# Performance work log

Measured on AMD Instinct MI355X. Metric: run time of the kernel, lower is better.

Reference implementation:

```python
import jax, jax.numpy as jnp
import numpy as np

# dims: T tokens, E experts, D model dim, F ffn dim, C per-expert capacity, K top-k routing
T, E, D, F, C, K = 4096, 8, 1024, 4096, 1536, 2


def setup_inputs() -> dict:
    key = jax.random.key(0)
    k_x, k_lg, k_w1, k_w2 = jax.random.split(key, 4)
    x = jax.random.normal(k_x, (T, D), jnp.float32)
    # external router: top-K of logits per token, softmax weights over kept logits
    logits = jax.random.normal(k_lg, (T, E), jnp.float32)
    topv, topi = jax.lax.top_k(logits, K)                      # (T,K)
    rows = jnp.arange(T)[:, None]
    route_mask = jnp.zeros((T, E), bool).at[rows, topi].set(True)
    route_weight = jnp.zeros((T, E), jnp.float32).at[rows, topi].set(
        jax.nn.softmax(topv, axis=-1))
    # stacked homogeneous expert MLP params (E leading axis, as in _stack_group)
    W1 = jax.random.normal(k_w1, (E, D, F), jnp.float32) / np.sqrt(D)
    b1 = jnp.zeros((E, F), jnp.float32)
    W2 = jax.random.normal(k_w2, (E, F, D), jnp.float32) / np.sqrt(F)
    b2 = jnp.zeros((E, D), jnp.float32)
    return dict(x=x, route_mask=route_mask, route_weight=route_weight,
                W1=W1, b1=b1, W2=W2, b2=b2)


def reference(x, route_mask, route_weight, W1, b1, W2, b2):
    """MoE with per-expert capacity: top-C tokens per expert by route weight,
    gather -> vmapped expert MLP -> weighted scatter-combine.
    Math identical to the one-hot slot einsums ('ect,t...->ec...' dispatch and
    'ecf,ect,te->tf' combine) of the original, expressed as gather/scatter.
    """
    Tn, En = route_mask.shape
    w_te = jnp.where(route_mask, route_weight, 0.0)            # (T,E)
    # per-expert scores; unrouted tokens get -inf so they can never be selected
    w_et = jnp.where(route_mask.T, w_te.T, -jnp.inf)           # (E,T)
    vals, idx = jax.lax.top_k(w_et, C)                         # (E,C) token ids per slot
    valid = jnp.isfinite(vals)                                  # slot actually filled
    # dispatch: gather token features into (E,C,D); empty slots are zero rows
    xe = x[idx] * valid[..., None]
    # grouped expert MLP (vmap over E via batched einsum)
    h = jax.nn.relu(jnp.einsum('ecd,edf->ecf', xe, W1) + b1[:, None, :])
    out = jnp.einsum('ecf,efd->ecd', h, W2) + b2[:, None, :]    # (E,C,D)
    # combine: y[t] = sum over slots assigned to t of w_te[t,e] * out[e,c]
    gain = jnp.where(valid, jnp.take_along_axis(w_te.T, idx, axis=1), 0.0)  # (E,C)
    y = jnp.zeros((Tn, out.shape[-1]), out.dtype)
    y = y.at[idx.reshape(-1)].add((out * gain[..., None]).reshape(-1, out.shape[-1]))
    return y
```

## Files before the change

kernel.cpp:

```cpp
#include <hip/hip_runtime.h>
#include <hip/hip_bf16.h>
#include <stdint.h>

#define T_TOK 4096
#define NE    8
#define DM    1024
#define FF    4096
#define CAP   1536

typedef __attribute__((ext_vector_type(8))) __bf16 bf16x8;
typedef __attribute__((ext_vector_type(4))) float  f32x4;

__device__ __forceinline__ void gload_lds16(const void* gptr, void* lptr) {
  __builtin_amdgcn_global_load_lds(
      (__attribute__((address_space(1))) void*)(uintptr_t)gptr,
      (__attribute__((address_space(3))) void*)(uintptr_t)lptr,
      16, 0, 0);
}


__global__ void conv_x_kernel(const float4* __restrict__ src, ushort4* __restrict__ dst, int n4) {
  int i = blockIdx.x * blockDim.x + threadIdx.x;
  if (i >= n4) return;
  float4 v = src[i];
  ushort4 o;
  o.x = __builtin_bit_cast(unsigned short, __float2bfloat16(v.x));
  o.y = __builtin_bit_cast(unsigned short, __float2bfloat16(v.y));
  o.z = __builtin_bit_cast(unsigned short, __float2bfloat16(v.z));
  o.w = __builtin_bit_cast(unsigned short, __float2bfloat16(v.w));
  dst[i] = o;
}

__global__ __launch_bounds__(256)
void tconv_kernel(const float* __restrict__ src, __hip_bfloat16* __restrict__ dst,
                  int R, int C) {
  __shared__ float tile[64][65];
  const int b  = blockIdx.z;
  const int r0 = blockIdx.y * 64;
  const int c0 = blockIdx.x * 64;
  const float* s = src + (size_t)b * R * C;
  __hip_bfloat16* d = dst + (size_t)b * R * C;
  const int tid = threadIdx.x;
  const int tx = tid & 63, ty = tid >> 6;
#pragma unroll
  for (int rr = ty; rr < 64; rr += 4)
    tile[rr][tx] = s[(size_t)(r0 + rr) * C + c0 + tx];
  __syncthreads();
  const int lg = tid & 15;
  const int cg = tid >> 4;
#pragma unroll
  for (int w = 0; w < 4; ++w) {
    const int cc = w * 16 + cg;
    const int r4 = lg * 4;
    ushort4 o;
    o.x = __builtin_bit_cast(unsigned short, __float2bfloat16(tile[r4 + 0][cc]));
    o.y = __builtin_bit_cast(unsigned short, __float2bfloat16(tile[r4 + 1][cc]));
    o.z = __builtin_bit_cast(unsigned short, __float2bfloat16(tile[r4 + 2][cc]));
    o.w = __builtin_bit_cast(unsigned short, __float2bfloat16(tile[r4 + 3][cc]));
    *(ushort4*)&d[(size_t)(c0 + cc) * R + r0 + r4] = o;
  }
}

__global__ void router_kernel(const float* __restrict__ rw, int* __restrict__ counts,
                              int* __restrict__ tok_ids, float* __restrict__ gains) {
  int t = blockIdx.x * blockDim.x + threadIdx.x;
  if (t >= T_TOK) return;
#pragma unroll
  for (int e = 0; e < NE; ++e) {
    float w = rw[t * NE + e];
    if (w > 0.f) {
      int pos = atomicAdd(&counts[e], 1);
      if (pos < CAP) {
        tok_ids[e * CAP + pos] = t;
        gains[e * CAP + pos]   = w;
      }
    }
  }
}

__global__ void pad_kernel(const int* __restrict__ counts, int* __restrict__ tok_ids,
                           float* __restrict__ gains) {
  int i = blockIdx.x * blockDim.x + threadIdx.x;
  if (i >= NE * CAP) return;
  int e = i / CAP, pos = i % CAP;
  int ne = min(counts[e], CAP);
  if (pos >= ne) { tok_ids[i] = 0; gains[i] = 0.f; }
}


template <int PASS>
__global__ __launch_bounds__(256, 3)
void moe_gemm(const __hip_bfloat16* __restrict__ Asrc,
              const __hip_bfloat16* __restrict__ Bsrc,
              const float* __restrict__ bias,
              const int* __restrict__ counts,
              const int* __restrict__ tok_ids,
              const float* __restrict__ gains,
              __hip_bfloat16* __restrict__ Hout,
              float* __restrict__ y)
{
  constexpr int K  = (PASS == 1) ? DM : FF;
  constexpr int NP = (PASS == 1) ? FF : DM;
  constexpr int MT = CAP / 128;
  constexpr int NT = NP / 128;
  constexpr int KT = K / 32;

  const int bid = blockIdx.x;
  const int e   = bid / (MT * NT);
  const int rem = bid % (MT * NT);
  const int mt  = rem / NT;
  const int nt  = rem % NT;

  const int Ne = min(counts[e], CAP);
  const int m0 = mt * 128;
  if (m0 >= Ne) return;
  const int n0 = nt * 128;

  __shared__ alignas(16) __hip_bfloat16 As[2 * 128 * 32];
  __shared__ alignas(16) __hip_bfloat16 Bs[2 * 128 * 32];

  const int tid  = threadIdx.x;
  const int lane = tid & 63;
  const int wid  = tid >> 6;
  const int wm   = wid >> 1;
  const int wn   = wid & 1;

  const int srow  = tid >> 2;
  const int cs    = ((tid & 3) ^ ((srow >> 1) & 3)) * 8;

  const __hip_bfloat16 *aptr0, *aptr1;
  if (PASS == 1) {
    const int tok0 = tok_ids[e * CAP + m0 + srow];
    const int tok1 = tok_ids[e * CAP + m0 + 64 + srow];
    aptr0 = Asrc + (size_t)tok0 * DM + cs;
    aptr1 = Asrc + (size_t)tok1 * DM + cs;
  } else {
    aptr0 = Asrc + ((size_t)e * CAP + m0 + srow) * FF + cs;
    aptr1 = Asrc + ((size_t)e * CAP + m0 + 64 + srow) * FF + cs;
  }
  const __hip_bfloat16* bptr0 = Bsrc + ((size_t)e * NP + n0 + srow) * K + cs;
  const __hip_bfloat16* bptr1 = Bsrc + ((size_t)e * NP + n0 + 64 + srow) * K + cs;

  char* AsB = (char*)As;
  char* BsB = (char*)Bs;
  const int fr = lane & 15;
  const int fq = lane >> 4;
  const int kbyte = ((fq ^ ((fr >> 1) & 3)) << 4);

  f32x4 acc[4][4] = {};

#define STAGE(buf, kt)                                                        \
  do {                                                                        \
    gload_lds16(aptr0 + (kt) * 32, AsB + (buf) * 8192 + wid * 1024);          \
    gload_lds16(aptr1 + (kt) * 32, AsB + (buf) * 8192 + 4096 + wid * 1024);   \
    gload_lds16(bptr0 + (kt) * 32, BsB + (buf) * 8192 + wid * 1024);          \
    gload_lds16(bptr1 + (kt) * 32, BsB + (buf) * 8192 + 4096 + wid * 1024);   \
  } while (0)

#define COMPUTE(buf)                                                          \
  do {                                                                        \
    const char* Ab = AsB + (buf) * 8192;                                      \
    const char* Bb = BsB + (buf) * 8192;                                      \
    bf16x8 af[4], bfr[4];                                                     \
    _Pragma("unroll") for (int i = 0; i < 4; ++i)                             \
        af[i] = *(const bf16x8*)(Ab + (wm * 64 + i * 16 + fr) * 64 + kbyte);  \
    _Pragma("unroll") for (int j = 0; j < 4; ++j)                             \
        bfr[j] = *(const bf16x8*)(Bb + (wn * 64 + j * 16 + fr) * 64 + kbyte); \
    _Pragma("unroll") for (int i = 0; i < 4; ++i)                             \
        _Pragma("unroll") for (int j = 0; j < 4; ++j)                         \
            acc[i][j] = __builtin_amdgcn_mfma_f32_16x16x32_bf16(              \
                af[i], bfr[j], acc[i][j], 0, 0, 0);                           \
  } while (0)

  STAGE(0, 0);
  int cur = 0;
  for (int kt = 0; kt + 1 < KT; ++kt) {
    STAGE(cur ^ 1, kt + 1);
    asm volatile("s_waitcnt vmcnt(4)" ::: "memory");
    __builtin_amdgcn_s_barrier();
    __builtin_amdgcn_sched_barrier(0);
    COMPUTE(cur);
    asm volatile("" ::: "memory");
    __builtin_amdgcn_s_barrier();
    cur ^= 1;
  }
  asm volatile("s_waitcnt vmcnt(0)" ::: "memory");
  __builtin_amdgcn_s_barrier();
  __builtin_amdgcn_sched_barrier(0);
  COMPUTE(cur);

#undef STAGE
#undef COMPUTE

  const int colb = n0 + wn * 64 + fr;
  if (PASS == 1) {
#pragma unroll
    for (int j = 0; j < 4; ++j) {
      const float bv = bias[(size_t)e * NP + colb + j * 16];
#pragma unroll
      for (int i = 0; i < 4; ++i)
#pragma unroll
        for (int rr = 0; rr < 4; ++rr) {
          const int row = m0 + wm * 64 + i * 16 + fq * 4 + rr;
          float v = acc[i][j][rr] + bv;
          v = v > 0.f ? v : 0.f;
          Hout[((size_t)e * CAP + row) * FF + colb + j * 16] = __float2bfloat16(v);
        }
    }
  } else {
    float bv[4];
#pragma unroll
    for (int j = 0; j < 4; ++j) bv[j] = bias[(size_t)e * NP + colb + j * 16];
#pragma unroll
    for (int i = 0; i < 4; ++i)
#pragma unroll
      for (int rr = 0; rr < 4; ++rr) {
        const int row  = m0 + wm * 64 + i * 16 + fq * 4 + rr;
        const int slot = e * CAP + row;
        const float g  = gains[slot];
        if (g != 0.f) {
          const int tok = tok_ids[slot];
          float* yrow = y + (size_t)tok * DM + colb;
#pragma unroll
          for (int j = 0; j < 4; ++j)
            atomicAdd(yrow + j * 16, (acc[i][j][rr] + bv[j]) * g);
        }
      }
  }
}


extern "C" void kernel_launch(void* const* d_in, const int* in_sizes, int n_in,
                              void* d_out, int out_size, void* d_ws, size_t ws_size,
                              hipStream_t stream) {
  const float* x  = (const float*)d_in[0];
  const float* rw = (const float*)d_in[2];
  const float* W1 = (const float*)d_in[3];
  const float* b1 = (const float*)d_in[4];
  const float* W2 = (const float*)d_in[5];
  const float* b2 = (const float*)d_in[6];
  float* y = (float*)d_out;

  char* ws = (char*)d_ws;
  size_t off = 0;
  auto alloc = [&](size_t bytes) {
    void* p = ws + off;
    off = (off + bytes + 255) & ~(size_t)255;
    return p;
  };
  __hip_bfloat16* xb  = (__hip_bfloat16*)alloc((size_t)T_TOK * DM * 2);
  __hip_bfloat16* w1t = (__hip_bfloat16*)alloc((size_t)NE * DM * FF * 2);
  __hip_bfloat16* w2t = (__hip_bfloat16*)alloc((size_t)NE * FF * DM * 2);
  __hip_bfloat16* Hb  = (__hip_bfloat16*)alloc((size_t)NE * CAP * FF * 2);
  int*   counts  = (int*)alloc(NE * sizeof(int));
  int*   tok_ids = (int*)alloc((size_t)NE * CAP * sizeof(int));
  float* gains   = (float*)alloc((size_t)NE * CAP * sizeof(float));
  (void)ws_size; (void)in_sizes; (void)n_in; (void)out_size;

  hipMemsetAsync(y, 0, (size_t)T_TOK * DM * sizeof(float), stream);
  hipMemsetAsync(counts, 0, NE * sizeof(int), stream);

  conv_x_kernel<<<(T_TOK * DM / 4 + 255) / 256, 256, 0, stream>>>(
      (const float4*)x, (ushort4*)xb, T_TOK * DM / 4);
  tconv_kernel<<<dim3(FF / 64, DM / 64, NE), 256, 0, stream>>>(W1, w1t, DM, FF);
  tconv_kernel<<<dim3(DM / 64, FF / 64, NE), 256, 0, stream>>>(W2, w2t, FF, DM);
  router_kernel<<<(T_TOK + 255) / 256, 256, 0, stream>>>(rw, counts, tok_ids, gains);
  pad_kernel<<<(NE * CAP + 255) / 256, 256, 0, stream>>>(counts, tok_ids, gains);

  moe_gemm<1><<<NE * (CAP / 128) * (FF / 128), 256, 0, stream>>>(
      xb, w1t, b1, counts, tok_ids, gains, Hb, nullptr);
  moe_gemm<2><<<NE * (CAP / 128) * (DM / 128), 256, 0, stream>>>(
      Hb, w2t, b2, counts, tok_ids, gains, nullptr, y);
}
```

Before: 351.9 us.

## Rewrite expert GEMMs as 256x256 8-wave tiles with phased LDS pipeline and split-K

Replaces the 128x128, 4-wave GEMM with 256x256 tiles computed by 512-thread blocks using 64-wide K steps. Each step is split into interleaved phases that overlap global-to-LDS staging with MFMA work, and MFMA sections run at raised priority. The block index is remapped into an XCD-aware order, and the second GEMM uses a 2-way split-K, with the bias added only by the first split. The goal is more operand reuse per byte loaded and better latency hiding. In exchange it uses 128KB of LDS per block, has fewer blocks at coarser granularity on capacity tails, and doubles atomic traffic in pass 2.

After: 368.0 us. 1.05x slower.

```diff
diff --git a/kernel.cpp b/kernel.cpp
--- a/kernel.cpp
+++ b/kernel.cpp
@@ -89,141 +89,176 @@
 
 
 template <int PASS>
-__global__ __launch_bounds__(256, 3)
-void moe_gemm(const __hip_bfloat16* __restrict__ Asrc,
-              const __hip_bfloat16* __restrict__ Bsrc,
-              const float* __restrict__ bias,
-              const int* __restrict__ counts,
-              const int* __restrict__ tok_ids,
-              const float* __restrict__ gains,
-              __hip_bfloat16* __restrict__ Hout,
-              float* __restrict__ y)
+__global__ __launch_bounds__(512, 2)
+void moe_gemm8(const __hip_bfloat16* __restrict__ Asrc,
+               const __hip_bfloat16* __restrict__ Bsrc,
+               const float* __restrict__ bias,
+               const int* __restrict__ counts,
+               const int* __restrict__ tok_ids,
+               const float* __restrict__ gains,
+               __hip_bfloat16* __restrict__ Hout,
+               float* __restrict__ y)
 {
-  constexpr int K  = (PASS == 1) ? DM : FF;
-  constexpr int NP = (PASS == 1) ? FF : DM;
-  constexpr int MT = CAP / 128;
-  constexpr int NT = NP / 128;
-  constexpr int KT = K / 32;
-
-  const int bid = blockIdx.x;
-  const int e   = bid / (MT * NT);
-  const int rem = bid % (MT * NT);
-  const int mt  = rem / NT;
-  const int nt  = rem % NT;
+  constexpr int K   = (PASS == 1) ? DM : FF;
+  constexpr int NP  = (PASS == 1) ? FF : DM;
+  constexpr int MT  = CAP / 256;
+  constexpr int NT  = NP / 256;
+  constexpr int SK  = (PASS == 1) ? 1 : 2;
+  constexpr int NWG = NE * MT * NT * SK;
+  constexpr int KP  = K / SK;
+  constexpr int KT  = KP / 64;
+  constexpr int KTM = KT - 1;
+  constexpr int NIT = KT / 2;
+
+  const int id = (blockIdx.x & 7) * (NWG / 8) + (blockIdx.x >> 3);
+  const int e  = id / (MT * NT * SK);
+  int r        = id % (MT * NT * SK);
+  const int sp = r / (MT * NT);
+  r            = r % (MT * NT);
+  const int nt = r / MT;
+  const int mt = r % MT;
 
   const int Ne = min(counts[e], CAP);
-  const int m0 = mt * 128;
+  const int m0 = mt * 256;
   if (m0 >= Ne) return;
-  const int n0 = nt * 128;
-
-  __shared__ alignas(16) __hip_bfloat16 As[2 * 128 * 32];
-  __shared__ alignas(16) __hip_bfloat16 Bs[2 * 128 * 32];
+  const int n0 = nt * 256;
+  const int k0 = sp * KP;
+
+  __shared__ alignas(128) char LDSmem[131072];
+  char* AsB = LDSmem;
+  char* BsB = LDSmem + 65536;
 
   const int tid  = threadIdx.x;
   const int lane = tid & 63;
   const int wid  = tid >> 6;
-  const int wm   = wid >> 1;
-  const int wn   = wid & 1;
-
-  const int srow  = tid >> 2;
-  const int cs    = ((tid & 3) ^ ((srow >> 1) & 3)) * 8;
-
-  const __hip_bfloat16 *aptr0, *aptr1;
+  const int wm   = wid >> 2;
+  const int wn   = wid & 3;
+  const int fr   = lane & 15;
+  const int fq   = lane >> 4;
+
+  const int sr  = tid >> 3;
+  const int kg  = tid & 7;
+  const int ksw = ((kg ^ (sr & 7)) << 4);
+
+  const char *aP[2][2], *bP[2][2];
+#pragma unroll
+  for (int h = 0; h < 2; ++h)
+#pragma unroll
+    for (int l = 0; l < 2; ++l) {
+      const int row = h * 128 + l * 64 + sr;
+      if (PASS == 1) {
+        const int tok = tok_ids[e * CAP + m0 + row];
+        aP[h][l] = (const char*)Asrc + ((size_t)tok * DM + k0) * 2 + ksw;
+      } else {
+        aP[h][l] = (const char*)Asrc + (((size_t)e * CAP + m0 + row) * FF + k0) * 2 + ksw;
+      }
+      bP[h][l] = (const char*)Bsrc + (((size_t)e * NP + n0 + row) * K + k0) * 2 + ksw;
+    }
+
+  const int kz0 = ((fq ^ (fr & 7)) << 4);
+  const int kz1 = (((4 + fq) ^ (fr & 7)) << 4);
+  const char* rdA0 = AsB + wm * 16384 + fr * 128 + kz0;
+  const char* rdA1 = AsB + wm * 16384 + fr * 128 + kz1;
+  const char* rdB0 = BsB + (wn >> 1) * 16384 + (wn & 1) * 8192 + fr * 128 + kz0;
+  const char* rdB1 = BsB + (wn >> 1) * 16384 + (wn & 1) * 8192 + fr * 128 + kz1;
+
+  f32x4  acc[8][4] = {};
+  bf16x8 bfr[4][2], af[2][2];
+
+#define STAGE_A(h, d, kt) do {                                                          \
+    gload_lds16(aP[h][0] + (kt) * 128, AsB + (d) * 32768 + (h) * 16384 + tid * 16);     \
+    gload_lds16(aP[h][1] + (kt) * 128, AsB + (d) * 32768 + (h) * 16384 + 8192 + tid * 16); \
+  } while (0)
+#define STAGE_B(h, d, kt) do {                                                          \
+    gload_lds16(bP[h][0] + (kt) * 128, BsB + (d) * 32768 + (h) * 16384 + tid * 16);     \
+    gload_lds16(bP[h][1] + (kt) * 128, BsB + (d) * 32768 + (h) * 16384 + 8192 + tid * 16); \
+  } while (0)
+#define VM4 asm volatile("s_waitcnt vmcnt(4)" ::: "memory")
+#define PHASE(d, q, LOADB, STG, VM) do {                                                \
+    if (LOADB) {                                                                        \
+      _Pragma("unroll") for (int j = 0; j < 4; ++j) {                                   \
+        bfr[j][0] = *(const bf16x8*)(rdB0 + (d) * 32768 + j * 2048);                    \
+        bfr[j][1] = *(const bf16x8*)(rdB1 + (d) * 32768 + j * 2048);                    \
+      }                                                                                 \
+    }                                                                                   \
+    af[0][0] = *(const bf16x8*)(rdA0 + (d) * 32768 + (q) * 4096);                       \
+    af[0][1] = *(const bf16x8*)(rdA1 + (d) * 32768 + (q) * 4096);                       \
+    af[1][0] = *(const bf16x8*)(rdA0 + (d) * 32768 + (q) * 4096 + 2048);                \
+    af[1][1] = *(const bf16x8*)(rdA1 + (d) * 32768 + (q) * 4096 + 2048);                \
+    STG;                                                                                \
+    asm volatile("s_barrier" ::: "memory");                                             \
+    asm volatile("s_waitcnt lgkmcnt(0)" ::: "memory");                                  \
+    __builtin_amdgcn_sched_barrier(0);                                                  \
+    __builtin_amdgcn_s_setprio(1);                                                      \
+    _Pragma("unroll") for (int f = 0; f < 2; ++f)                                       \
+      _Pragma("unroll") for (int j = 0; j < 4; ++j) {                                   \
+        acc[(q) * 2 + f][j] = __builtin_amdgcn_mfma_f32_16x16x32_bf16(                  \
+            af[f][0], bfr[j][0], acc[(q) * 2 + f][j], 0, 0, 0);                         \
+        acc[(q) * 2 + f][j] = __builtin_amdgcn_mfma_f32_16x16x32_bf16(                  \
+            af[f][1], bfr[j][1], acc[(q) * 2 + f][j], 0, 0, 0);                         \
+      }                                                                                 \
+    __builtin_amdgcn_s_setprio(0);                                                      \
+    __builtin_amdgcn_sched_barrier(0);                                                  \
+    VM;                                                                                 \
+    asm volatile("s_barrier" ::: "memory");                                             \
+  } while (0)
+
+  STAGE_B(0, 0, 0); STAGE_B(1, 0, 0); STAGE_A(0, 0, 0); STAGE_A(1, 0, 0);
+  STAGE_B(0, 1, 1); STAGE_B(1, 1, 1);
+  asm volatile("s_waitcnt vmcnt(4)" ::: "memory");
+  asm volatile("s_barrier" ::: "memory");
+
+#pragma unroll 1
+  for (int it = 0; it < NIT; ++it) {
+    const int ta = 2 * it + 1;
+    const int tb = (2 * it + 2) & KTM;
+    const int tc = (2 * it + 3) & KTM;
+    PHASE(0, 0, true,  STAGE_A(0, 1, ta), (void)0);
+    PHASE(0, 1, false, STAGE_A(1, 1, ta), (void)0);
+    PHASE(0, 2, false, STAGE_B(0, 0, tb), (void)0);
+    PHASE(0, 3, false, STAGE_B(1, 0, tb), VM4);
+    PHASE(1, 0, true,  STAGE_A(0, 0, tb), (void)0);
+    PHASE(1, 1, false, STAGE_A(1, 0, tb), (void)0);
+    PHASE(1, 2, false, STAGE_B(0, 1, tc), (void)0);
+    PHASE(1, 3, false, STAGE_B(1, 1, tc), VM4);
+  }
+#undef STAGE_A
+#undef STAGE_B
+#undef VM4
+#undef PHASE
+
   if (PASS == 1) {
-    const int tok0 = tok_ids[e * CAP + m0 + srow];
-    const int tok1 = tok_ids[e * CAP + m0 + 64 + srow];
-    aptr0 = Asrc + (size_t)tok0 * DM + cs;
-    aptr1 = Asrc + (size_t)tok1 * DM + cs;
-  } else {
-    aptr0 = Asrc + ((size_t)e * CAP + m0 + srow) * FF + cs;
-    aptr1 = Asrc + ((size_t)e * CAP + m0 + 64 + srow) * FF + cs;
-  }
-  const __hip_bfloat16* bptr0 = Bsrc + ((size_t)e * NP + n0 + srow) * K + cs;
-  const __hip_bfloat16* bptr1 = Bsrc + ((size_t)e * NP + n0 + 64 + srow) * K + cs;
-
-  char* AsB = (char*)As;
-  char* BsB = (char*)Bs;
-  const int fr = lane & 15;
-  const int fq = lane >> 4;
-  const int kbyte = ((fq ^ ((fr >> 1) & 3)) << 4);
-
-  f32x4 acc[4][4] = {};
-
-#define STAGE(buf, kt)                                                        \
-  do {                                                                        \
-    gload_lds16(aptr0 + (kt) * 32, AsB + (buf) * 8192 + wid * 1024);          \
-    gload_lds16(aptr1 + (kt) * 32, AsB + (buf) * 8192 + 4096 + wid * 1024);   \
-    gload_lds16(bptr0 + (kt) * 32, BsB + (buf) * 8192 + wid * 1024);          \
-    gload_lds16(bptr1 + (kt) * 32, BsB + (buf) * 8192 + 4096 + wid * 1024);   \
-  } while (0)
-
-#define COMPUTE(buf)                                                          \
-  do {                                                                        \
-    const char* Ab = AsB + (buf) * 8192;                                      \
-    const char* Bb = BsB + (buf) * 8192;                                      \
-    bf16x8 af[4], bfr[4];                                                     \
-    _Pragma("unroll") for (int i = 0; i < 4; ++i)                             \
-        af[i] = *(const bf16x8*)(Ab + (wm * 64 + i * 16 + fr) * 64 + kbyte);  \
-    _Pragma("unroll") for (int j = 0; j < 4; ++j)                             \
-        bfr[j] = *(const bf16x8*)(Bb + (wn * 64 + j * 16 + fr) * 64 + kbyte); \
-    _Pragma("unroll") for (int i = 0; i < 4; ++i)                             \
-        _Pragma("unroll") for (int j = 0; j < 4; ++j)                         \
-            acc[i][j] = __builtin_amdgcn_mfma_f32_16x16x32_bf16(              \
-                af[i], bfr[j], acc[i][j], 0, 0, 0);                           \
-  } while (0)
-
-  STAGE(0, 0);
-  int cur = 0;
-  for (int kt = 0; kt + 1 < KT; ++kt) {
-    STAGE(cur ^ 1, kt + 1);
-    asm volatile("s_waitcnt vmcnt(4)" ::: "memory");
-    __builtin_amdgcn_s_barrier();
-    __builtin_amdgcn_sched_barrier(0);
-    COMPUTE(cur);
-    asm volatile("" ::: "memory");
-    __builtin_amdgcn_s_barrier();
-    cur ^= 1;
-  }
-  asm volatile("s_waitcnt vmcnt(0)" ::: "memory");
-  __builtin_amdgcn_s_barrier();
-  __builtin_amdgcn_sched_barrier(0);
-  COMPUTE(cur);
-
-#undef STAGE
-#undef COMPUTE
-
-  const int colb = n0 + wn * 64 + fr;
-  if (PASS == 1) {
-#pragma unroll
-    for (int j = 0; j < 4; ++j) {
-      const float bv = bias[(size_t)e * NP + colb + j * 16];
-#pragma unroll
-      for (int i = 0; i < 4; ++i)
+#pragma unroll
+    for (int nj = 0; nj < 4; ++nj) {
+      const int col = n0 + wn * 64 + nj * 16 + fr;
+      const float bv = bias[e * NP + col];
+#pragma unroll
+      for (int mi = 0; mi < 8; ++mi)
 #pragma unroll
         for (int rr = 0; rr < 4; ++rr) {
-          const int row = m0 + wm * 64 + i * 16 + fq * 4 + rr;
-          float v = acc[i][j][rr] + bv;
-          v = v > 0.f ? v : 0.f;
-          Hout[((size_t)e * CAP + row) * FF + colb + j * 16] = __float2bfloat16(v);
+          const int row = m0 + wm * 128 + mi * 16 + fq * 4 + rr;
+          float v = acc[mi][nj][rr] + bv;
+          Hout[((size_t)e * CAP + row) * FF + col] = __float2bfloat16(v > 0.f ? v : 0.f);
         }
     }
   } else {
     float bv[4];
 #pragma unroll
-    for (int j = 0; j < 4; ++j) bv[j] = bias[(size_t)e * NP + colb + j * 16];
-#pragma unroll
-    for (int i = 0; i < 4; ++i)
+    for (int nj = 0; nj < 4; ++nj)
+      bv[nj] = (sp == 0) ? bias[e * NP + n0 + wn * 64 + nj * 16 + fr] : 0.f;
+#pragma unroll
+    for (int mi = 0; mi < 8; ++mi)
 #pragma unroll
       for (int rr = 0; rr < 4; ++rr) {
-        const int row  = m0 + wm * 64 + i * 16 + fq * 4 + rr;
+        const int row  = m0 + wm * 128 + mi * 16 + fq * 4 + rr;
         const int slot = e * CAP + row;
         const float g  = gains[slot];
         if (g != 0.f) {
           const int tok = tok_ids[slot];
-          float* yrow = y + (size_t)tok * DM + colb;
-#pragma unroll
-          for (int j = 0; j < 4; ++j)
-            atomicAdd(yrow + j * 16, (acc[i][j][rr] + bv[j]) * g);
+          float* yrow = y + (size_t)tok * DM + n0 + wn * 64 + fr;
+#pragma unroll
+          for (int nj = 0; nj < 4; ++nj)
+            atomicAdd(yrow + nj * 16, (acc[mi][nj][rr] + bv[nj]) * g);
         }
       }
   }
@@ -267,8 +302,8 @@
   router_kernel<<<(T_TOK + 255) / 256, 256, 0, stream>>>(rw, counts, tok_ids, gains);
   pad_kernel<<<(NE * CAP + 255) / 256, 256, 0, stream>>>(counts, tok_ids, gains);
 
-  moe_gemm<1><<<NE * (CAP / 128) * (FF / 128), 256, 0, stream>>>(
+  moe_gemm8<1><<<NE * (CAP / 256) * (FF / 256), 512, 0, stream>>>(
       xb, w1t, b1, counts, tok_ids, gains, Hb, nullptr);
-  moe_gemm<2><<<NE * (CAP / 128) * (DM / 128), 256, 0, stream>>>(
+  moe_gemm8<2><<<NE * (CAP / 256) * (DM / 256) * 2, 512, 0, stream>>>(
       Hb, w2t, b2, counts, tok_ids, gains, nullptr, y);
 }
```
